# Performance work log

Measured on AMD Instinct MI355X. Metric: run time of the kernel, lower is better.

Reference implementation:

```python
import jax, jax.numpy as jnp
import numpy as np

B, S, HID = 4, 1024, 2048
NH, NKV = 32, 8
HD = HID // NH  # 64
N_REP = NH // NKV
THETA = 10000.0


def _rope_cos_sin(position_ids, head_dim, dtype):
    inv_freq = 1.0 / (THETA ** (jnp.arange(0, head_dim, 2, dtype=jnp.float32) / head_dim))
    ang = position_ids.astype(jnp.float32)[:, None] * inv_freq[None, :]  # [S, HD/2]
    emb = jnp.concatenate([ang, ang], axis=-1)  # [S, HD]
    return jnp.cos(emb).astype(dtype), jnp.sin(emb).astype(dtype)


def _rotate_half(x):
    x1, x2 = jnp.split(x, 2, axis=-1)
    return jnp.concatenate([-x2, x1], axis=-1)


def setup_inputs() -> dict:
    key = jax.random.key(0)
    ks = jax.random.split(key, 6)
    scale = 0.02
    hidden_states = jax.random.normal(ks[0], (B, S, HID), dtype=jnp.float32)
    # causal additive mask
    neg = jnp.finfo(jnp.float32).min
    causal = jnp.where(jnp.tril(jnp.ones((S, S), dtype=bool)), 0.0, neg)
    attention_mask = causal[None, None, :, :].astype(jnp.float32)
    position_ids = jnp.arange(S, dtype=jnp.int32)
    Wq = jax.random.normal(ks[1], (HID, NH * HD), dtype=jnp.float32) * scale
    Wk = jax.random.normal(ks[2], (HID, NKV * HD), dtype=jnp.float32) * scale
    Wv = jax.random.normal(ks[3], (HID, NKV * HD), dtype=jnp.float32) * scale
    Wo = jax.random.normal(ks[4], (NH * HD, HID), dtype=jnp.float32) * scale
    return {"hidden_states": hidden_states, "attention_mask": attention_mask,
            "position_ids": position_ids, "Wq": Wq, "Wk": Wk, "Wv": Wv, "Wo": Wo}


def reference(hidden_states, attention_mask, position_ids, Wq, Wk, Wv, Wo):
    b, s, _ = hidden_states.shape
    dtype = hidden_states.dtype
    q = (hidden_states @ Wq).reshape(b, s, NH, HD).transpose(0, 2, 1, 3)   # [B,NH,S,HD]
    k = (hidden_states @ Wk).reshape(b, s, NKV, HD).transpose(0, 2, 1, 3)  # [B,NKV,S,HD]
    v = (hidden_states @ Wv).reshape(b, s, NKV, HD).transpose(0, 2, 1, 3)
    # RoPE
    cos, sin = _rope_cos_sin(position_ids, HD, dtype)  # [S,HD]
    cos = cos[None, None, :, :]
    sin = sin[None, None, :, :]
    q = q * cos + _rotate_half(q) * sin
    k = k * cos + _rotate_half(k) * sin
    # repeat KV heads to match query heads
    k = jnp.repeat(k, N_REP, axis=1)  # [B,NH,S,HD]
    v = jnp.repeat(v, N_REP, axis=1)
    scale = HD ** -0.5
    attn = jnp.einsum('bhqd,bhkd->bhqk', q, k) * scale + attention_mask
    attn = jax.nn.softmax(attn.astype(jnp.float32), axis=-1).astype(dtype)
    out = jnp.einsum('bhqk,bhkd->bhqd', attn, v)  # [B,NH,S,HD]
    out = out.transpose(0, 2, 1, 3).reshape(b, s, NH * HD)
    return out @ Wo
```

## Files before the change

kernel.cpp:

```cpp
#include <hip/hip_runtime.h>
#include <hip/hip_bf16.h>
#include <math.h>

typedef __bf16 bf16_t;
typedef __bf16 bf16x4 __attribute__((ext_vector_type(4)));
typedef __bf16 bf16x8 __attribute__((ext_vector_type(8)));
typedef float f32x4 __attribute__((ext_vector_type(4)));

#define MFMA_BF16(a, b, c) __builtin_amdgcn_mfma_f32_16x16x32_bf16((a), (b), (c), 0, 0, 0)

__device__ __forceinline__ void gload_lds16(const void* g, void* s) {
  __builtin_amdgcn_global_load_lds((const __attribute__((address_space(1))) void*)g,
                                   (__attribute__((address_space(3))) void*)s, 16, 0, 0);
}

__device__ __forceinline__ bf16x8 lds_frag(const bf16_t* base, int row, int k) {
  const char* p = reinterpret_cast<const char*>(base) + row * 128 + ((((k >> 3) ^ (row & 7)) << 4));
  return *reinterpret_cast<const bf16x8*>(p);
}

__global__ __launch_bounds__(256) void k_prep(const float* __restrict__ X, bf16_t* __restrict__ Xb,
                                              const float* __restrict__ Wq, const float* __restrict__ Wk,
                                              const float* __restrict__ Wv, bf16_t* __restrict__ Wqkv,
                                              const float* __restrict__ Wo, bf16_t* __restrict__ Wot) {
  const int bid = blockIdx.x;
  const int tid = threadIdx.x;
  if (bid < 4096) {
    const int i = bid * 256 + tid;
    const float4* X4 = reinterpret_cast<const float4*>(X);
    const float4 a = X4[2 * i], c = X4[2 * i + 1];
    bf16x8 v;
    v[0] = (bf16_t)a.x; v[1] = (bf16_t)a.y; v[2] = (bf16_t)a.z; v[3] = (bf16_t)a.w;
    v[4] = (bf16_t)c.x; v[5] = (bf16_t)c.y; v[6] = (bf16_t)c.z; v[7] = (bf16_t)c.w;
    reinterpret_cast<bf16x8*>(Xb)[i] = v;
    return;
  }
  __shared__ bf16_t t[64][65];
  const float* W;
  bf16_t* Wt;
  int N, nl0, n0, k0, Kdim;
  if (bid < 5632) {
    const int tq = bid - 4096;
    n0 = (tq % 48) * 64; k0 = (tq / 48) * 64; Kdim = 2048;
    if (n0 < 2048)      { W = Wq; N = 2048; nl0 = n0; }
    else if (n0 < 2560) { W = Wk; N = 512;  nl0 = n0 - 2048; }
    else                { W = Wv; N = 512;  nl0 = n0 - 2560; }
    Wt = Wqkv;
  } else {
    const int to = bid - 5632;
    n0 = (to % 32) * 64; k0 = (to / 32) * 64; Kdim = 2048;
    W = Wo; N = 2048; nl0 = n0; Wt = Wot;
  }
#pragma unroll
  for (int i = 0; i < 16; ++i) {
    const int idx = i * 256 + tid;
    const int kl = idx >> 6, nl = idx & 63;
    t[nl][kl] = (bf16_t)W[(size_t)(k0 + kl) * N + nl0 + nl];
  }
  __syncthreads();
#pragma unroll
  for (int i = 0; i < 16; ++i) {
    const int idx = i * 256 + tid;
    const int nl = idx >> 6, kl = idx & 63;
    Wt[(size_t)(n0 + nl) * Kdim + k0 + kl] = t[nl][kl];
  }
}

__global__ __launch_bounds__(512) void k_gemm_qkv(const bf16_t* __restrict__ A,
                                                  const bf16_t* __restrict__ Bt,
                                                  const int* __restrict__ pos_ids,
                                                  bf16_t* __restrict__ Qb,
                                                  bf16_t* __restrict__ Kb,
                                                  bf16_t* __restrict__ Vt) {
  constexpr int K = 2048;
  constexpr int NT = K / 64;
  __shared__ __align__(16) char smem[139264];
  const int tid = threadIdx.x;
  const int w = tid >> 6, l = tid & 63;
  const int g = l >> 4, ln = l & 15;
  const int orig = blockIdx.y * 16 + blockIdx.x;
  const int swz = (orig & 7) * 32 + (orig >> 3);
  const int m0 = (swz >> 4) * 256, n0 = (swz & 15) * 192;
  const int csrc = ((l & 7) ^ (l >> 3)) * 8;
  const int rowbase = m0 + w * 32;

  auto STAGE_A = [&](int slot, int half, int kt) {
    char* base = smem + slot * 32768 + w * 4096 + half * 2048;
    const bf16_t* gs = A + (size_t)(m0 + w * 32 + half * 16 + (l >> 3)) * K + kt + csrc;
    gload_lds16(gs, base);
    gload_lds16(gs + (size_t)8 * K, base + 1024);
  };
  auto STAGE_B = [&](int slot, int j, int kt) {
    char* base = smem + 65536 + slot * 24576 + w * 3072 + j * 1024;
    const bf16_t* gs = Bt + (size_t)(n0 + w * 24 + j * 8 + (l >> 3)) * K + kt + csrc;
    gload_lds16(gs, base);
  };
  auto FRAG = [&](const char* base, int row, int kk) -> bf16x8 {
    return *reinterpret_cast<const bf16x8*>(base + row * 128 + ((((kk >> 3) ^ (row & 7)) << 4)));
  };

  const f32x4 zero4 = {0.f, 0.f, 0.f, 0.f};
  f32x4 acc[2][12];
#pragma unroll
  for (int i = 0; i < 2; ++i)
#pragma unroll
    for (int j = 0; j < 12; ++j) acc[i][j] = zero4;

  STAGE_A(0, 0, 0); STAGE_A(0, 1, 0);
  STAGE_B(0, 0, 0); STAGE_B(0, 1, 0); STAGE_B(0, 2, 0);
  STAGE_B(1, 0, 64); STAGE_B(1, 1, 64); STAGE_B(1, 2, 64);
  asm volatile("s_waitcnt vmcnt(3)" ::: "memory");
  __builtin_amdgcn_sched_barrier(0);
  __builtin_amdgcn_s_barrier();
  __builtin_amdgcn_sched_barrier(0);

  for (int t = 0; t < NT; ++t) {
    const int as = t & 1;
    const int bs = t % 3;
    const int bs2 = (t + 2) % 3;
    const char* Abase = smem + as * 32768;
    const char* Bbase = smem + 65536 + bs * 24576;

    bf16x8 aA[2][2];
#pragma unroll
    for (int e = 0; e < 2; ++e)
#pragma unroll
      for (int kh = 0; kh < 2; ++kh)
        aA[e][kh] = FRAG(Abase, w * 32 + e * 16 + ln, kh * 32 + g * 8);
    bf16x8 bB0[6][2];
#pragma unroll
    for (int fc = 0; fc < 6; ++fc)
#pragma unroll
      for (int kh = 0; kh < 2; ++kh)
        bB0[fc][kh] = FRAG(Bbase, fc * 16 + ln, kh * 32 + g * 8);
    if (t + 1 < NT) { STAGE_A(as ^ 1, 0, (t + 1) * 64); STAGE_A(as ^ 1, 1, (t + 1) * 64); }
    __builtin_amdgcn_sched_barrier(0);
    __builtin_amdgcn_s_barrier();
    __builtin_amdgcn_sched_barrier(0);
    __builtin_amdgcn_s_setprio(1);
#pragma unroll
    for (int e = 0; e < 2; ++e)
#pragma unroll
      for (int fc = 0; fc < 6; ++fc)
#pragma unroll
        for (int kh = 0; kh < 2; ++kh)
          acc[e][fc] = MFMA_BF16(aA[e][kh], bB0[fc][kh], acc[e][fc]);
    __builtin_amdgcn_s_setprio(0);
    __builtin_amdgcn_sched_barrier(0);
    __builtin_amdgcn_s_barrier();
    __builtin_amdgcn_sched_barrier(0);

    bf16x8 bB1[6][2];
#pragma unroll
    for (int fc = 0; fc < 6; ++fc)
#pragma unroll
      for (int kh = 0; kh < 2; ++kh)
        bB1[fc][kh] = FRAG(Bbase, (6 + fc) * 16 + ln, kh * 32 + g * 8);
    if (t + 2 < NT) { STAGE_B(bs2, 0, (t + 2) * 64); STAGE_B(bs2, 1, (t + 2) * 64); STAGE_B(bs2, 2, (t + 2) * 64); }
    if (t >= NT - 2) asm volatile("s_waitcnt vmcnt(0)" ::: "memory");
    else             asm volatile("s_waitcnt vmcnt(3)" ::: "memory");
    __builtin_amdgcn_sched_barrier(0);
    __builtin_amdgcn_s_barrier();
    __builtin_amdgcn_sched_barrier(0);
    __builtin_amdgcn_s_setprio(1);
#pragma unroll
    for (int e = 0; e < 2; ++e)
#pragma unroll
      for (int fc = 0; fc < 6; ++fc)
#pragma unroll
        for (int kh = 0; kh < 2; ++kh)
          acc[e][6 + fc] = MFMA_BF16(aA[e][kh], bB1[fc][kh], acc[e][6 + fc]);
    __builtin_amdgcn_s_setprio(0);
    __builtin_amdgcn_sched_barrier(0);
    __builtin_amdgcn_s_barrier();
    __builtin_amdgcn_sched_barrier(0);
  }

  const float if0 = exp2f(-(float)ln * 0.4152410118609203f);
  const float if1 = exp2f(-(float)(ln + 16) * 0.4152410118609203f);
  const float QS = 0.125f * 1.4426950408889634f;

#pragma unroll
  for (int gg = 0; gg < 3; ++gg) {
    const int colg = n0 + gg * 64;
    if (colg < 2560) {
      const bool isQ = (colg < 2048);
      bf16_t* out = isQ ? (Qb + (size_t)(colg >> 6) * 1024 * 64)
                        : (Kb + (size_t)((colg - 2048) >> 6) * 1024 * 64);
      const size_t bstride = isQ ? (size_t)32 * 1024 * 64 : (size_t)8 * 1024 * 64;
      const float sc = isQ ? QS : 1.0f;
#pragma unroll
      for (int i = 0; i < 2; ++i)
#pragma unroll
        for (int r = 0; r < 4; ++r) {
          const int row = rowbase + i * 16 + g * 4 + r;
          const int b = row >> 10, s = row & 1023;
          const float pos = (float)pos_ids[s];
          float sn0, cs0, sn1, cs1;
          __sincosf(pos * if0, &sn0, &cs0);
          __sincosf(pos * if1, &sn1, &cs1);
          const float x0 = acc[i][gg * 4 + 0][r], x1 = acc[i][gg * 4 + 1][r];
          const float x2 = acc[i][gg * 4 + 2][r], x3 = acc[i][gg * 4 + 3][r];
          const float o0 = (x0 * cs0 - x2 * sn0) * sc;
          const float o2 = (x2 * cs0 + x0 * sn0) * sc;
          const float o1 = (x1 * cs1 - x3 * sn1) * sc;
          const float o3 = (x3 * cs1 + x1 * sn1) * sc;
          bf16_t* p = out + (size_t)b * bstride + (size_t)s * 64;
          p[ln] = (bf16_t)o0;
          p[16 + ln] = (bf16_t)o1;
          p[32 + ln] = (bf16_t)o2;
          p[48 + ln] = (bf16_t)o3;
        }
    } else {
      const int kh = (colg - 2560) >> 6;
#pragma unroll
      for (int i = 0; i < 2; ++i)
#pragma unroll
        for (int r = 0; r < 4; ++r) {
          const int row = rowbase + i * 16 + g * 4 + r;
          const int b = row >> 10, s = row & 1023;
          const size_t vb = ((size_t)(b * 8 + kh) * 64) * 1024;
#pragma unroll
          for (int fcl = 0; fcl < 4; ++fcl) {
            const int d = fcl * 16 + ln;
            Vt[vb + (size_t)d * 1024 + s] = (bf16_t)acc[i][gg * 4 + fcl][r];
          }
        }
    }
  }
}

__global__ __launch_bounds__(512) void k_gemm2(const bf16_t* __restrict__ A,
                                               const bf16_t* __restrict__ Bt,
                                               float* __restrict__ C) {
  constexpr int K = 2048;
  constexpr int NT = K / 64;
  constexpr int N = 2048;
  __shared__ __align__(16) char smem[98304];
  const int tid = threadIdx.x;
  const int w = tid >> 6, l = tid & 63;
  const int g = l >> 4, ln = l & 15;
  const int orig = blockIdx.y * 8 + blockIdx.x;
  const int swz = (orig & 7) * 32 + (orig >> 3);
  const int m0 = (swz >> 3) * 128, n0 = (swz & 7) * 256;
  const int csrc = ((l & 7) ^ (l >> 3)) * 8;
  const int srow = w * 16 + (l >> 3);

  auto STAGE_A = [&](int slot, int kt) {
    char* base = smem + slot * 16384 + w * 2048;
    const bf16_t* gs = A + (size_t)(m0 + srow) * K + kt + csrc;
    gload_lds16(gs, base);
    gload_lds16(gs + (size_t)8 * K, base + 1024);
  };
  auto STAGE_B = [&](int slot, int h, int kt) {
    char* base = smem + 32768 + slot * 32768 + h * 16384 + w * 2048;
    const bf16_t* gs = Bt + (size_t)(n0 + h * 128 + srow) * K + kt + csrc;
    gload_lds16(gs, base);
    gload_lds16(gs + (size_t)8 * K, base + 1024);
  };
  auto FRAG = [&](const char* half, int row, int kk) -> bf16x8 {
    return *reinterpret_cast<const bf16x8*>(half + row * 128 + ((((kk >> 3) ^ (row & 7)) << 4)));
  };

  const f32x4 zero4 = {0.f, 0.f, 0.f, 0.f};
  f32x4 acc[8][2];
#pragma unroll
  for (int i = 0; i < 8; ++i)
#pragma unroll
    for (int j = 0; j < 2; ++j) acc[i][j] = zero4;

  STAGE_A(0, 0);
  STAGE_B(0, 0, 0); STAGE_B(0, 1, 0);
  STAGE_B(1, 0, 64); STAGE_B(1, 1, 64);
  asm volatile("s_waitcnt vmcnt(4)" ::: "memory");
  __builtin_amdgcn_sched_barrier(0);
  __builtin_amdgcn_s_barrier();
  __builtin_amdgcn_sched_barrier(0);

  const int brow = w * 32;
  for (int t = 0; t < NT; ++t) {
    const int s = t & 1;
    const char* Ah = smem + s * 16384;
    const char* Bh = smem + 32768 + s * 32768 + (brow >> 7) * 16384;
    const int rb = brow & 127;
    bf16x8 bB[2][2];
#pragma unroll
    for (int q = 0; q < 4; ++q) {
      if (q == 0) {
#pragma unroll
        for (int fc = 0; fc < 2; ++fc)
#pragma unroll
          for (int kh = 0; kh < 2; ++kh) bB[fc][kh] = FRAG(Bh, rb + fc * 16 + ln, kh * 32 + g * 8);
      }
      bf16x8 aA[2][2];
#pragma unroll
      for (int e = 0; e < 2; ++e)
#pragma unroll
        for (int kh = 0; kh < 2; ++kh) aA[e][kh] = FRAG(Ah, (q * 2 + e) * 16 + ln, kh * 32 + g * 8);
      if (q == 0 && t + 1 < NT) STAGE_A(s ^ 1, (t + 1) * 64);
      if (q == 1 && t + 2 < NT) STAGE_B(s, 0, (t + 2) * 64);
      if (q == 2 && t + 2 < NT) STAGE_B(s, 1, (t + 2) * 64);
      if (q == 3) {
        if (t >= NT - 2) asm volatile("s_waitcnt vmcnt(0)" ::: "memory");
        else             asm volatile("s_waitcnt vmcnt(4)" ::: "memory");
      }
      __builtin_amdgcn_sched_barrier(0);
      __builtin_amdgcn_s_barrier();
      __builtin_amdgcn_sched_barrier(0);
      __builtin_amdgcn_s_setprio(1);
#pragma unroll
      for (int e = 0; e < 2; ++e)
#pragma unroll
        for (int fc = 0; fc < 2; ++fc)
#pragma unroll
          for (int kh = 0; kh < 2; ++kh)
            acc[q * 2 + e][fc] = MFMA_BF16(aA[e][kh], bB[fc][kh], acc[q * 2 + e][fc]);
      __builtin_amdgcn_s_setprio(0);
      __builtin_amdgcn_sched_barrier(0);
      __builtin_amdgcn_s_barrier();
      __builtin_amdgcn_sched_barrier(0);
    }
  }

#pragma unroll
  for (int i = 0; i < 8; ++i)
#pragma unroll
    for (int fc = 0; fc < 2; ++fc)
#pragma unroll
      for (int r = 0; r < 4; ++r) {
        const int row = m0 + i * 16 + g * 4 + r;
        const int col = n0 + brow + fc * 16 + ln;
        C[(size_t)row * N + col] = acc[i][fc][r];
      }
}

__global__ __launch_bounds__(512) void k_attn(const bf16_t* __restrict__ Qb,
                                              const bf16_t* __restrict__ Kb,
                                              const bf16_t* __restrict__ Vt,
                                              bf16_t* __restrict__ AO) {
  __shared__ bf16_t Ks[3][64 * 64];
  __shared__ bf16_t Vs[3][64 * 64];
  __shared__ bf16_t Ps[8][32 * 64];
  const int tid = threadIdx.x;
  const int w = tid >> 6, l = tid & 63;
  const int g = l >> 4, ln = l & 15;
  const int lr = l >> 3;
  const int csrc = ((l & 7) ^ lr) * 8;
  const int f = blockIdx.x;
  const int y = blockIdx.y;
  const int b = y >> 3, kh = y & 7;
  const int h = kh * 4 + (w >> 1);
  const int rh = (w & 1) * 32;
  const int qAw = f * 64 + rh, qBw = (15 - f) * 64 + rh;
  const bf16_t* Qh = Qb + (size_t)(b * 32 + h) * 1024 * 64;
  const bf16_t* Kh = Kb + (size_t)(b * 8 + kh) * 1024 * 64;
  const bf16_t* Vh = Vt + (size_t)(b * 8 + kh) * 64 * 1024;

  bf16x8 aqA[2][2], aqB[2][2];
#pragma unroll
  for (int fr = 0; fr < 2; ++fr) {
    aqA[fr][0] = *reinterpret_cast<const bf16x8*>(Qh + (size_t)(qAw + fr * 16 + ln) * 64 + g * 8);
    aqA[fr][1] = *reinterpret_cast<const bf16x8*>(Qh + (size_t)(qAw + fr * 16 + ln) * 64 + 32 + g * 8);
    aqB[fr][0] = *reinterpret_cast<const bf16x8*>(Qh + (size_t)(qBw + fr * 16 + ln) * 64 + g * 8);
    aqB[fr][1] = *reinterpret_cast<const bf16x8*>(Qh + (size_t)(qBw + fr * 16 + ln) * 64 + 32 + g * 8);
  }

  const f32x4 zero4 = {0.f, 0.f, 0.f, 0.f};
  const f32x4 shift4 = {-16.f, -16.f, -16.f, -16.f};
  f32x4 oA[2][4], oB[2][4];
#pragma unroll
  for (int fr = 0; fr < 2; ++fr)
#pragma unroll
    for (int d = 0; d < 4; ++d) { oA[fr][d] = zero4; oB[fr][d] = zero4; }
  float lA[2][4], lB[2][4];
#pragma unroll
  for (int fr = 0; fr < 2; ++fr)
#pragma unroll
    for (int r = 0; r < 4; ++r) { lA[fr][r] = 0.f; lB[fr][r] = 0.f; }

  auto STAGE = [&](int buf, int kt) {
    gload_lds16(Kh + (size_t)(kt * 64 + w * 8 + lr) * 64 + csrc, &Ks[buf][w * 512]);
    gload_lds16(Vh + (size_t)(w * 8 + lr) * 1024 + kt * 64 + csrc, &Vs[buf][w * 512]);
  };

  auto ACT = [&](const bf16x8 (&aq)[2][2], f32x4 (&o)[2][4], float (&lr_)[2][4],
                 int qw0, bool dg, int kt, const bf16_t* Kc, const bf16_t* Vc) {
    bf16x8 kf[4][2];
#pragma unroll
    for (int nb = 0; nb < 4; ++nb) {
      kf[nb][0] = lds_frag(Kc, nb * 16 + ln, g * 8);
      kf[nb][1] = lds_frag(Kc, nb * 16 + ln, 32 + g * 8);
    }
    f32x4 sc[2][4];
#pragma unroll
    for (int fr = 0; fr < 2; ++fr)
#pragma unroll
      for (int nb = 0; nb < 4; ++nb) {
        f32x4 z = shift4;
        z = MFMA_BF16(aq[fr][0], kf[nb][0], z);
        sc[fr][nb] = MFMA_BF16(aq[fr][1], kf[nb][1], z);
      }
#pragma unroll
    for (int fr = 0; fr < 2; ++fr)
#pragma unroll
      for (int r = 0; r < 4; ++r) {
        const int qrow = qw0 + fr * 16 + g * 4 + r;
        float rs = 0.f;
#pragma unroll
        for (int nb = 0; nb < 4; ++nb) {
          float v = sc[fr][nb][r];
          if (dg && (kt * 64 + nb * 16 + ln) > qrow) v = -INFINITY;
          const float p = exp2f(v);
          sc[fr][nb][r] = p;
          rs += p;
        }
        lr_[fr][r] += rs;
      }

    char* pw = reinterpret_cast<char*>(&Ps[w][0]);
#pragma unroll
    for (int fr = 0; fr < 2; ++fr)
#pragma unroll
      for (int r = 0; r < 4; ++r) {
        const int q = fr * 16 + g * 4 + r;
        const int sw = (q & 7) << 4;
#pragma unroll
        for (int nb = 0; nb < 4; ++nb) {
          const int byte = q * 128 + ((nb * 16 + ln) * 2);
          *reinterpret_cast<bf16_t*>(pw + (byte ^ sw)) = (bf16_t)sc[fr][nb][r];
        }
      }
    asm volatile("s_waitcnt lgkmcnt(0)" ::: "memory");

    bf16x8 vf[4][2];
#pragma unroll
    for (int d = 0; d < 4; ++d) {
      vf[d][0] = lds_frag(Vc, d * 16 + ln, g * 8);
      vf[d][1] = lds_frag(Vc, d * 16 + ln, 32 + g * 8);
    }
#pragma unroll
    for (int fr = 0; fr < 2; ++fr) {
      const bf16x8 pa0 = lds_frag(&Ps[w][0], fr * 16 + ln, g * 8);
      const bf16x8 pa1 = lds_frag(&Ps[w][0], fr * 16 + ln, 32 + g * 8);
#pragma unroll
      for (int d = 0; d < 4; ++d) {
        o[fr][d] = MFMA_BF16(pa0, vf[d][0], o[fr][d]);
        o[fr][d] = MFMA_BF16(pa1, vf[d][1], o[fr][d]);
      }
    }
  };

  const int nA = f + 1;
  auto TILE = [&](int u) { return (u < nA) ? u : u - nA; };

  STAGE(0, TILE(0));
  STAGE(1, TILE(1));

  for (int t = 0; t < 17; ++t) {
    if (t < 16) asm volatile("s_waitcnt vmcnt(2)" ::: "memory");
    else        asm volatile("s_waitcnt vmcnt(0)" ::: "memory");
    __builtin_amdgcn_sched_barrier(0);
    __builtin_amdgcn_s_barrier();
    __builtin_amdgcn_sched_barrier(0);
    if (t + 2 < 17) STAGE((t + 2) % 3, TILE(t + 2));
    const bf16_t* Kc = &Ks[t % 3][0];
    const bf16_t* Vc = &Vs[t % 3][0];
    if (t < nA) ACT(aqA, oA, lA, qAw, t == nA - 1, t, Kc, Vc);
    else        ACT(aqB, oB, lB, qBw, t == 16, t - nA, Kc, Vc);
  }

  auto EPI = [&](f32x4 (&o)[2][4], float (&lr_)[2][4], int qw0) {
#pragma unroll
    for (int fr = 0; fr < 2; ++fr)
#pragma unroll
      for (int r = 0; r < 4; ++r) {
        float rs = lr_[fr][r];
        rs += __shfl_xor(rs, 1);
        rs += __shfl_xor(rs, 2);
        rs += __shfl_xor(rs, 4);
        rs += __shfl_xor(rs, 8);
        const float inv = 1.0f / rs;
        const int srow = qw0 + fr * 16 + g * 4 + r;
        const size_t base = ((size_t)(b * 1024 + srow)) * 2048 + h * 64;
#pragma unroll
        for (int d = 0; d < 4; ++d) AO[base + d * 16 + ln] = (bf16_t)(o[fr][d][r] * inv);
      }
  };
  EPI(oA, lA, qAw);
  EPI(oB, lB, qBw);
}

extern "C" void kernel_launch(void* const* d_in, const int* in_sizes, int n_in,
                              void* d_out, int out_size, void* d_ws, size_t ws_size,
                              hipStream_t stream) {
  const float* X = (const float*)d_in[0];
  const int* pos = (const int*)d_in[2];
  const float* Wq = (const float*)d_in[3];
  const float* Wk = (const float*)d_in[4];
  const float* Wv = (const float*)d_in[5];
  const float* Wo = (const float*)d_in[6];
  float* out = (float*)d_out;
  char* ws = (char*)d_ws;

  bf16_t* Xb   = (bf16_t*)(ws);
  bf16_t* Wqkv = (bf16_t*)(ws + 16777216);
  bf16_t* Wot  = (bf16_t*)(ws + 29360128);
  bf16_t* Qb   = (bf16_t*)(ws + 62914560);
  bf16_t* Kb   = (bf16_t*)(ws + 79691776);
  bf16_t* Vt   = (bf16_t*)(ws + 83886080);
  bf16_t* AO   = (bf16_t*)(ws + 37748736);

  k_prep<<<6656, 256, 0, stream>>>(X, Xb, Wq, Wk, Wv, Wqkv, Wo, Wot);
  k_gemm_qkv<<<dim3(16, 16), 512, 0, stream>>>(Xb, Wqkv, pos, Qb, Kb, Vt);
  k_attn<<<dim3(8, 32), 512, 0, stream>>>(Qb, Kb, Vt, AO);
  k_gemm2<<<dim3(8, 32), 512, 0, stream>>>(AO, Wot, out);
}
```

Before: 158.9 us.

## Compute transposed S^T tiles and pass P via cross-lane shuffles instead of LDS

New measurement: 163.1 us. 1.03x slower.

```diff
diff --git a/kernel.cpp b/kernel.cpp
--- a/kernel.cpp
+++ b/kernel.cpp
@@ -6,6 +6,7 @@
 typedef __bf16 bf16x4 __attribute__((ext_vector_type(4)));
 typedef __bf16 bf16x8 __attribute__((ext_vector_type(8)));
 typedef float f32x4 __attribute__((ext_vector_type(4)));
+typedef unsigned int u32x4 __attribute__((ext_vector_type(4)));
 
 #define MFMA_BF16(a, b, c) __builtin_amdgcn_mfma_f32_16x16x32_bf16((a), (b), (c), 0, 0, 0)
 
@@ -17,6 +18,12 @@
 __device__ __forceinline__ bf16x8 lds_frag(const bf16_t* base, int row, int k) {
   const char* p = reinterpret_cast<const char*>(base) + row * 128 + ((((k >> 3) ^ (row & 7)) << 4));
   return *reinterpret_cast<const bf16x8*>(p);
+}
+
+__device__ __forceinline__ unsigned pk2(float a, float b) {
+  const unsigned short ua = __builtin_bit_cast(unsigned short, (bf16_t)a);
+  const unsigned short ub = __builtin_bit_cast(unsigned short, (bf16_t)b);
+  return (unsigned)ua | ((unsigned)ub << 16);
 }
 
 __global__ __launch_bounds__(256) void k_prep(const float* __restrict__ X, bf16_t* __restrict__ Xb,
@@ -340,7 +347,7 @@
                                               bf16_t* __restrict__ AO) {
   __shared__ bf16_t Ks[3][64 * 64];
   __shared__ bf16_t Vs[3][64 * 64];
-  __shared__ bf16_t Ps[8][32 * 64];
+  __shared__ bf16_t Pe[8][16 * 72];
   const int tid = threadIdx.x;
   const int w = tid >> 6, l = tid & 63;
   const int g = l >> 4, ln = l & 15;
@@ -372,80 +379,75 @@
   for (int fr = 0; fr < 2; ++fr)
 #pragma unroll
     for (int d = 0; d < 4; ++d) { oA[fr][d] = zero4; oB[fr][d] = zero4; }
-  float lA[2][4], lB[2][4];
-#pragma unroll
-  for (int fr = 0; fr < 2; ++fr)
-#pragma unroll
-    for (int r = 0; r < 4; ++r) { lA[fr][r] = 0.f; lB[fr][r] = 0.f; }
+  float lsA[2] = {0.f, 0.f}, lsB[2] = {0.f, 0.f};
+
+  const int srcA_lane = 32 * (g & 1) + ln;
+  const int srcB_lane = srcA_lane + 16;
+  const bool hi = (g >> 1) != 0;
 
   auto STAGE = [&](int buf, int kt) {
     gload_lds16(Kh + (size_t)(kt * 64 + w * 8 + lr) * 64 + csrc, &Ks[buf][w * 512]);
     gload_lds16(Vh + (size_t)(w * 8 + lr) * 1024 + kt * 64 + csrc, &Vs[buf][w * 512]);
   };
 
-  auto ACT = [&](const bf16x8 (&aq)[2][2], f32x4 (&o)[2][4], float (&lr_)[2][4],
+  auto ACT = [&](const bf16x8 (&aq)[2][2], f32x4 (&o)[2][4], float (&ls)[2],
                  int qw0, bool dg, int kt, const bf16_t* Kc, const bf16_t* Vc) {
-    bf16x8 kf[4][2];
+    bf16x8 kf[4][2], vf[4][2];
 #pragma unroll
     for (int nb = 0; nb < 4; ++nb) {
       kf[nb][0] = lds_frag(Kc, nb * 16 + ln, g * 8);
       kf[nb][1] = lds_frag(Kc, nb * 16 + ln, 32 + g * 8);
+      vf[nb][0] = lds_frag(Vc, nb * 16 + ln, g * 8);
+      vf[nb][1] = lds_frag(Vc, nb * 16 + ln, 32 + g * 8);
     }
-    f32x4 sc[2][4];
-#pragma unroll
-    for (int fr = 0; fr < 2; ++fr)
+#pragma unroll
+    for (int fr = 0; fr < 2; ++fr) {
+      f32x4 sc[4];
 #pragma unroll
       for (int nb = 0; nb < 4; ++nb) {
         f32x4 z = shift4;
-        z = MFMA_BF16(aq[fr][0], kf[nb][0], z);
-        sc[fr][nb] = MFMA_BF16(aq[fr][1], kf[nb][1], z);
-      }
-#pragma unroll
-    for (int fr = 0; fr < 2; ++fr)
-#pragma unroll
-      for (int r = 0; r < 4; ++r) {
-        const int qrow = qw0 + fr * 16 + g * 4 + r;
-        float rs = 0.f;
-#pragma unroll
-        for (int nb = 0; nb < 4; ++nb) {
-          float v = sc[fr][nb][r];
-          if (dg && (kt * 64 + nb * 16 + ln) > qrow) v = -INFINITY;
+        z = MFMA_BF16(kf[nb][0], aq[fr][0], z);
+        sc[nb] = MFMA_BF16(kf[nb][1], aq[fr][1], z);
+      }
+      const int qabs = qw0 + fr * 16 + ln;
+      float rs = 0.f;
+      unsigned dw0[4], dw1[4];
+#pragma unroll
+      for (int nb = 0; nb < 4; ++nb) {
+#pragma unroll
+        for (int r = 0; r < 4; ++r) {
+          float v = sc[nb][r];
+          if (dg && (kt * 64 + nb * 16 + g * 4 + r) > qabs) v = -INFINITY;
           const float p = exp2f(v);
-          sc[fr][nb][r] = p;
+          sc[nb][r] = p;
           rs += p;
         }
-        lr_[fr][r] += rs;
-      }
-
-    char* pw = reinterpret_cast<char*>(&Ps[w][0]);
-#pragma unroll
-    for (int fr = 0; fr < 2; ++fr)
-#pragma unroll
-      for (int r = 0; r < 4; ++r) {
-        const int q = fr * 16 + g * 4 + r;
-        const int sw = (q & 7) << 4;
-#pragma unroll
-        for (int nb = 0; nb < 4; ++nb) {
-          const int byte = q * 128 + ((nb * 16 + ln) * 2);
-          *reinterpret_cast<bf16_t*>(pw + (byte ^ sw)) = (bf16_t)sc[fr][nb][r];
-        }
-      }
-    asm volatile("s_waitcnt lgkmcnt(0)" ::: "memory");
-
-    bf16x8 vf[4][2];
-#pragma unroll
-    for (int d = 0; d < 4; ++d) {
-      vf[d][0] = lds_frag(Vc, d * 16 + ln, g * 8);
-      vf[d][1] = lds_frag(Vc, d * 16 + ln, 32 + g * 8);
-    }
-#pragma unroll
-    for (int fr = 0; fr < 2; ++fr) {
-      const bf16x8 pa0 = lds_frag(&Ps[w][0], fr * 16 + ln, g * 8);
-      const bf16x8 pa1 = lds_frag(&Ps[w][0], fr * 16 + ln, 32 + g * 8);
-#pragma unroll
-      for (int d = 0; d < 4; ++d) {
-        o[fr][d] = MFMA_BF16(pa0, vf[d][0], o[fr][d]);
-        o[fr][d] = MFMA_BF16(pa1, vf[d][1], o[fr][d]);
+        dw0[nb] = pk2(sc[nb][0], sc[nb][1]);
+        dw1[nb] = pk2(sc[nb][2], sc[nb][3]);
+      }
+      ls[fr] += rs;
+      bf16x8 pb[2];
+#pragma unroll
+      for (int kh2 = 0; kh2 < 2; ++kh2) {
+        const unsigned a0l = __shfl(dw0[2 * kh2], srcA_lane, 64);
+        const unsigned a1l = __shfl(dw1[2 * kh2], srcA_lane, 64);
+        const unsigned b0l = __shfl(dw0[2 * kh2], srcB_lane, 64);
+        const unsigned b1l = __shfl(dw1[2 * kh2], srcB_lane, 64);
+        const unsigned a0h = __shfl(dw0[2 * kh2 + 1], srcA_lane, 64);
+        const unsigned a1h = __shfl(dw1[2 * kh2 + 1], srcA_lane, 64);
+        const unsigned b0h = __shfl(dw0[2 * kh2 + 1], srcB_lane, 64);
+        const unsigned b1h = __shfl(dw1[2 * kh2 + 1], srcB_lane, 64);
+        u32x4 tv;
+        tv[0] = hi ? a0h : a0l;
+        tv[1] = hi ? a1h : a1l;
+        tv[2] = hi ? b0h : b0l;
+        tv[3] = hi ? b1h : b1l;
+        pb[kh2] = __builtin_bit_cast(bf16x8, tv);
+      }
+#pragma unroll
+      for (int dblk = 0; dblk < 4; ++dblk) {
+        o[fr][dblk] = MFMA_BF16(vf[dblk][0], pb[0], o[fr][dblk]);
+        o[fr][dblk] = MFMA_BF16(vf[dblk][1], pb[1], o[fr][dblk]);
       }
     }
   };
@@ -465,29 +467,40 @@
     if (t + 2 < 17) STAGE((t + 2) % 3, TILE(t + 2));
     const bf16_t* Kc = &Ks[t % 3][0];
     const bf16_t* Vc = &Vs[t % 3][0];
-    if (t < nA) ACT(aqA, oA, lA, qAw, t == nA - 1, t, Kc, Vc);
-    else        ACT(aqB, oB, lB, qBw, t == 16, t - nA, Kc, Vc);
-  }
-
-  auto EPI = [&](f32x4 (&o)[2][4], float (&lr_)[2][4], int qw0) {
-#pragma unroll
-    for (int fr = 0; fr < 2; ++fr)
+    if (t < nA) ACT(aqA, oA, lsA, qAw, t == nA - 1, t, Kc, Vc);
+    else        ACT(aqB, oB, lsB, qBw, t == 16, t - nA, Kc, Vc);
+  }
+
+  bf16_t* pe = &Pe[w][0];
+  auto EPI = [&](f32x4 (&o)[2][4], float (&ls)[2], int qw0) {
+#pragma unroll
+    for (int fr = 0; fr < 2; ++fr) {
+      float s = ls[fr];
+      s += __shfl_xor(s, 16);
+      s += __shfl_xor(s, 32);
+      const float inv = 1.0f / s;
+      asm volatile("s_waitcnt lgkmcnt(0)" ::: "memory");
+      __builtin_amdgcn_sched_barrier(0);
+#pragma unroll
+      for (int dblk = 0; dblk < 4; ++dblk)
+#pragma unroll
+        for (int r = 0; r < 4; ++r)
+          pe[ln * 72 + dblk * 16 + g * 4 + r] = (bf16_t)(o[fr][dblk][r] * inv);
+      asm volatile("s_waitcnt lgkmcnt(0)" ::: "memory");
+      __builtin_amdgcn_sched_barrier(0);
+      const size_t rowb = (size_t)(b * 1024 + qw0 + fr * 16);
 #pragma unroll
       for (int r = 0; r < 4; ++r) {
-        float rs = lr_[fr][r];
-        rs += __shfl_xor(rs, 1);
-        rs += __shfl_xor(rs, 2);
-        rs += __shfl_xor(rs, 4);
-        rs += __shfl_xor(rs, 8);
-        const float inv = 1.0f / rs;
-        const int srow = qw0 + fr * 16 + g * 4 + r;
-        const size_t base = ((size_t)(b * 1024 + srow)) * 2048 + h * 64;
-#pragma unroll
-        for (int d = 0; d < 4; ++d) AO[base + d * 16 + ln] = (bf16_t)(o[fr][d][r] * inv);
-      }
-  };
-  EPI(oA, lA, qAw);
-  EPI(oB, lB, qBw);
+        const int q = g * 4 + r;
+        const size_t base = (rowb + q) * 2048 + h * 64;
+#pragma unroll
+        for (int dblk = 0; dblk < 4; ++dblk)
+          AO[base + dblk * 16 + ln] = pe[q * 72 + dblk * 16 + ln];
+      }
+    }
+  };
+  EPI(oA, lsA, qAw);
+  EPI(oB, lsB, qBw);
 }
 
 extern "C" void kernel_launch(void* const* d_in, const int* in_sizes, int n_in,
```

## Re-tile QKV GEMM warps as 4x2 grid to cut LDS B-fragment reads

Applied to the files above, without the earlier changes.

New measurement: 158.5 us. About the same (-0.2%).

```diff
diff --git a/kernel.cpp b/kernel.cpp
--- a/kernel.cpp
+++ b/kernel.cpp
@@ -78,11 +78,17 @@
   const int tid = threadIdx.x;
   const int w = tid >> 6, l = tid & 63;
   const int g = l >> 4, ln = l & 15;
+  const int wm = w >> 1, wn = w & 1;
   const int orig = blockIdx.y * 16 + blockIdx.x;
   const int swz = (orig & 7) * 32 + (orig >> 3);
   const int m0 = (swz >> 4) * 256, n0 = (swz & 15) * 192;
   const int csrc = ((l & 7) ^ (l >> 3)) * 8;
-  const int rowbase = m0 + w * 32;
+
+  const int fcs[6] = {wn ? 5 : 0, wn ? 7 : 1, wn ? 8 : 2,
+                      wn ? 9 : 3, wn ? 10 : 4, wn ? 11 : 6};
+  const int pLo[3] = {0, wn ? 2 : 1, wn ? 3 : 4};
+  const int pHi[3] = {wn ? 1 : 2, wn ? 4 : 3, 5};
+  const int pFc[3] = {wn ? 5 : 0, wn ? 8 : 1, wn ? 9 : 4};
 
   auto STAGE_A = [&](int slot, int half, int kt) {
     char* base = smem + slot * 32768 + w * 4096 + half * 2048;
@@ -100,11 +106,11 @@
   };
 
   const f32x4 zero4 = {0.f, 0.f, 0.f, 0.f};
-  f32x4 acc[2][12];
-#pragma unroll
-  for (int i = 0; i < 2; ++i)
-#pragma unroll
-    for (int j = 0; j < 12; ++j) acc[i][j] = zero4;
+  f32x4 acc[4][6];
+#pragma unroll
+  for (int i = 0; i < 4; ++i)
+#pragma unroll
+    for (int j = 0; j < 6; ++j) acc[i][j] = zero4;
 
   STAGE_A(0, 0, 0); STAGE_A(0, 1, 0);
   STAGE_B(0, 0, 0); STAGE_B(0, 1, 0); STAGE_B(0, 2, 0);
@@ -121,41 +127,41 @@
     const char* Abase = smem + as * 32768;
     const char* Bbase = smem + 65536 + bs * 24576;
 
-    bf16x8 aA[2][2];
-#pragma unroll
-    for (int e = 0; e < 2; ++e)
+    bf16x8 aA[4][2];
+#pragma unroll
+    for (int e = 0; e < 4; ++e)
 #pragma unroll
       for (int kh = 0; kh < 2; ++kh)
-        aA[e][kh] = FRAG(Abase, w * 32 + e * 16 + ln, kh * 32 + g * 8);
-    bf16x8 bB0[6][2];
-#pragma unroll
-    for (int fc = 0; fc < 6; ++fc)
+        aA[e][kh] = FRAG(Abase, wm * 64 + e * 16 + ln, kh * 32 + g * 8);
+    bf16x8 bB0[3][2];
+#pragma unroll
+    for (int a = 0; a < 3; ++a)
 #pragma unroll
       for (int kh = 0; kh < 2; ++kh)
-        bB0[fc][kh] = FRAG(Bbase, fc * 16 + ln, kh * 32 + g * 8);
+        bB0[a][kh] = FRAG(Bbase, fcs[a] * 16 + ln, kh * 32 + g * 8);
     if (t + 1 < NT) { STAGE_A(as ^ 1, 0, (t + 1) * 64); STAGE_A(as ^ 1, 1, (t + 1) * 64); }
     __builtin_amdgcn_sched_barrier(0);
     __builtin_amdgcn_s_barrier();
     __builtin_amdgcn_sched_barrier(0);
     __builtin_amdgcn_s_setprio(1);
 #pragma unroll
-    for (int e = 0; e < 2; ++e)
-#pragma unroll
-      for (int fc = 0; fc < 6; ++fc)
+    for (int e = 0; e < 4; ++e)
+#pragma unroll
+      for (int a = 0; a < 3; ++a)
 #pragma unroll
         for (int kh = 0; kh < 2; ++kh)
-          acc[e][fc] = MFMA_BF16(aA[e][kh], bB0[fc][kh], acc[e][fc]);
+          acc[e][a] = MFMA_BF16(aA[e][kh], bB0[a][kh], acc[e][a]);
     __builtin_amdgcn_s_setprio(0);
     __builtin_amdgcn_sched_barrier(0);
     __builtin_amdgcn_s_barrier();
     __builtin_amdgcn_sched_barrier(0);
 
-    bf16x8 bB1[6][2];
-#pragma unroll
-    for (int fc = 0; fc < 6; ++fc)
+    bf16x8 bB1[3][2];
+#pragma unroll
+    for (int a = 0; a < 3; ++a)
 #pragma unroll
       for (int kh = 0; kh < 2; ++kh)
-        bB1[fc][kh] = FRAG(Bbase, (6 + fc) * 16 + ln, kh * 32 + g * 8);
+        bB1[a][kh] = FRAG(Bbase, fcs[3 + a] * 16 + ln, kh * 32 + g * 8);
     if (t + 2 < NT) { STAGE_B(bs2, 0, (t + 2) * 64); STAGE_B(bs2, 1, (t + 2) * 64); STAGE_B(bs2, 2, (t + 2) * 64); }
     if (t >= NT - 2) asm volatile("s_waitcnt vmcnt(0)" ::: "memory");
     else             asm volatile("s_waitcnt vmcnt(3)" ::: "memory");
@@ -164,12 +170,12 @@
     __builtin_amdgcn_sched_barrier(0);
     __builtin_amdgcn_s_setprio(1);
 #pragma unroll
-    for (int e = 0; e < 2; ++e)
-#pragma unroll
-      for (int fc = 0; fc < 6; ++fc)
+    for (int e = 0; e < 4; ++e)
+#pragma unroll
+      for (int a = 0; a < 3; ++a)
 #pragma unroll
         for (int kh = 0; kh < 2; ++kh)
-          acc[e][6 + fc] = MFMA_BF16(aA[e][kh], bB1[fc][kh], acc[e][6 + fc]);
+          acc[e][3 + a] = MFMA_BF16(aA[e][kh], bB1[a][kh], acc[e][3 + a]);
     __builtin_amdgcn_s_setprio(0);
     __builtin_amdgcn_sched_barrier(0);
     __builtin_amdgcn_s_barrier();
@@ -181,50 +187,42 @@
   const float QS = 0.125f * 1.4426950408889634f;
 
 #pragma unroll
-  for (int gg = 0; gg < 3; ++gg) {
-    const int colg = n0 + gg * 64;
-    if (colg < 2560) {
-      const bool isQ = (colg < 2048);
-      bf16_t* out = isQ ? (Qb + (size_t)(colg >> 6) * 1024 * 64)
-                        : (Kb + (size_t)((colg - 2048) >> 6) * 1024 * 64);
+  for (int p = 0; p < 3; ++p) {
+    const int aLo = pLo[p], aHi = pHi[p], fcLo = pFc[p];
+    const int colhead = n0 + (fcLo >> 2) * 64;
+    const float ifr = (fcLo & 1) ? if1 : if0;
+    const int dLo = (fcLo & 3) * 16 + ln;
+    if (colhead < 2560) {
+      const bool isQ = (colhead < 2048);
+      bf16_t* out = isQ ? (Qb + (size_t)(colhead >> 6) * 1024 * 64)
+                        : (Kb + (size_t)((colhead - 2048) >> 6) * 1024 * 64);
       const size_t bstride = isQ ? (size_t)32 * 1024 * 64 : (size_t)8 * 1024 * 64;
-      const float sc = isQ ? QS : 1.0f;
-#pragma unroll
-      for (int i = 0; i < 2; ++i)
+      const float sc_ = isQ ? QS : 1.0f;
+#pragma unroll
+      for (int e = 0; e < 4; ++e)
 #pragma unroll
         for (int r = 0; r < 4; ++r) {
-          const int row = rowbase + i * 16 + g * 4 + r;
+          const int row = m0 + wm * 64 + e * 16 + g * 4 + r;
           const int b = row >> 10, s = row & 1023;
           const float pos = (float)pos_ids[s];
-          float sn0, cs0, sn1, cs1;
-          __sincosf(pos * if0, &sn0, &cs0);
-          __sincosf(pos * if1, &sn1, &cs1);
-          const float x0 = acc[i][gg * 4 + 0][r], x1 = acc[i][gg * 4 + 1][r];
-          const float x2 = acc[i][gg * 4 + 2][r], x3 = acc[i][gg * 4 + 3][r];
-          const float o0 = (x0 * cs0 - x2 * sn0) * sc;
-          const float o2 = (x2 * cs0 + x0 * sn0) * sc;
-          const float o1 = (x1 * cs1 - x3 * sn1) * sc;
-          const float o3 = (x3 * cs1 + x1 * sn1) * sc;
-          bf16_t* p = out + (size_t)b * bstride + (size_t)s * 64;
-          p[ln] = (bf16_t)o0;
-          p[16 + ln] = (bf16_t)o1;
-          p[32 + ln] = (bf16_t)o2;
-          p[48 + ln] = (bf16_t)o3;
+          float sn, cs;
+          __sincosf(pos * ifr, &sn, &cs);
+          const float xlo = acc[e][aLo][r], xhi = acc[e][aHi][r];
+          bf16_t* pp = out + (size_t)b * bstride + (size_t)s * 64;
+          pp[dLo]      = (bf16_t)((xlo * cs - xhi * sn) * sc_);
+          pp[dLo + 32] = (bf16_t)((xhi * cs + xlo * sn) * sc_);
         }
     } else {
-      const int kh = (colg - 2560) >> 6;
-#pragma unroll
-      for (int i = 0; i < 2; ++i)
+      const int kh = (colhead - 2560) >> 6;
+#pragma unroll
+      for (int e = 0; e < 4; ++e)
 #pragma unroll
         for (int r = 0; r < 4; ++r) {
-          const int row = rowbase + i * 16 + g * 4 + r;
+          const int row = m0 + wm * 64 + e * 16 + g * 4 + r;
           const int b = row >> 10, s = row & 1023;
           const size_t vb = ((size_t)(b * 8 + kh) * 64) * 1024;
-#pragma unroll
-          for (int fcl = 0; fcl < 4; ++fcl) {
-            const int d = fcl * 16 + ln;
-            Vt[vb + (size_t)d * 1024 + s] = (bf16_t)acc[i][gg * 4 + fcl][r];
-          }
+          Vt[vb + (size_t)dLo * 1024 + s]        = (bf16_t)acc[e][aLo][r];
+          Vt[vb + (size_t)(dLo + 32) * 1024 + s] = (bf16_t)acc[e][aHi][r];
         }
     }
   }
```
